# Performance work log

Hardware: AMD Instinct MI355X
Metric: run time of the kernel (lower is better)

## Reference

```python
import jax, jax.numpy as jnp
import numpy as np

K = 3            # kernel_size
ZETA = 1e-3      # crf_zeta
NUM_ITER = 2     # crf_num_iter
TOL = 0.0        # tolerance


def unfold3(x):
    """torch.nn.Unfold(3, stride=1, padding=1): [B,C,H,W] -> [B,C,9,H*W].
    Channel-major, kernel positions row-major (matches torch ordering)."""
    B, C, H, W = x.shape
    xp = jnp.pad(x, ((0, 0), (0, 0), (1, 1), (1, 1)))
    patches = jnp.stack(
        [xp[:, :, i:i + H, j:j + W] for i in range(K) for j in range(K)], axis=2
    )  # [B,C,9,H,W]
    return patches.reshape(B, C, K * K, H * W)


def setup_inputs() -> dict:
    key = jax.random.key(0)
    k1, k2, k3 = jax.random.split(key, 3)
    B, C, H, W, D = 2, 3, 256, 704, 64
    # scale color to O(zeta) so the gaussian affinity kernel is non-degenerate
    color = jax.random.normal(k1, (B, C, H, W), dtype=jnp.float32) * ZETA
    feats = jax.random.normal(k2, (B, C, H, W), dtype=jnp.float32)  # unused by forward, kept for signature fidelity
    logits = jax.random.normal(k3, (B, D, H, W), dtype=jnp.float32)
    ws = jnp.full((1,), 0.015, dtype=jnp.float32)  # learned weight self.ws[0]
    return {"color": color, "feats": feats, "logits": logits, "ws": ws}


def reference(color, feats, logits, ws):
    B, C, H, W = color.shape
    D = logits.shape[1]
    HW = H * W

    # gaussian affinity kernel from guide image: [B, 9, HW]
    uc = unfold3(color)  # [B,C,9,HW]
    kernel = jnp.exp(-(((uc - color.reshape(B, C, 1, HW)) ** 2)
                       / (2.0 * ZETA ** 2)).sum(1))

    # label compatibility matrix miu: [D, D]
    idx = jnp.arange(D)
    miu = jnp.clip(jnp.abs(idx[:, None] - idx[None, :]).astype(jnp.float32) - TOL, 0.0)

    logits_flat = logits.reshape(B, D, HW)
    q = jax.nn.softmax(logits, axis=1)
    for _ in range(NUM_ITER):
        uq = unfold3(q)  # [B,D,9,HW]
        q_tilde = (uq * kernel[:, None]).sum(2) * ws  # [B,D,HW]
        q_hat = jnp.einsum('de,ben->bdn', miu, q_tilde)  # [B,D,HW]
        q = jax.nn.softmax(logits_flat - q_hat, axis=1).reshape(B, D, H, W)
    return q
```

## Files before the change

kernel.cpp:

```cpp
#include <hip/hip_runtime.h>
#include <hip/hip_fp16.h>

#define HH 256
#define WW 704
#define DD 64
#define CC 3
#define BB 2
#define HWN (HH * WW)

#define TY 8
#define TX 16
#define RY0 12
#define RX0 20
#define NP0 (RY0 * RX0)
#define RY1 10
#define RX1 18
#define NP1 (RY1 * RX1)
#define NTX (WW / TX)
#define NTY (HH / TY)
#define NTILES (NTX * NTY)

static constexpr float INV2Z2 = 1.0f / (2.0f * 1e-3f * 1e-3f);
static constexpr float LOG2E  = 1.4426950408889634f;

__device__ __forceinline__ float fexp2(float x) {
#if __has_builtin(__builtin_amdgcn_exp2f)
    return __builtin_amdgcn_exp2f(x);
#else
    return __expf(x * 0.6931471805599453f);
#endif
}

__global__ __launch_bounds__(256) void affinity_kernel(
    const float* __restrict__ color, const float* __restrict__ wsp,
    float* __restrict__ kaffp)
{
    int n = blockIdx.x * 256 + threadIdx.x;
    int b = blockIdx.y;
    int h = n / WW, w = n - h * WW;
    float wsv = wsp[0] * LOG2E;

    const float* cb = color + (size_t)b * CC * HWN + n;
    float c0 = cb[0], c1 = cb[HWN], c2 = cb[2 * HWN];
    bool hm = h > 0, hp = h < HH - 1, wm = w > 0, wp = w < WW - 1;

    float kk[9];
#pragma unroll
    for (int dh = -1; dh <= 1; ++dh) {
#pragma unroll
        for (int dw = -1; dw <= 1; ++dw) {
            int k = (dh + 1) * 3 + (dw + 1);
            bool valid = (dh < 0 ? hm : (dh > 0 ? hp : true)) &&
                         (dw < 0 ? wm : (dw > 0 ? wp : true));
            int off = valid ? (dh * WW + dw) : 0;
            float u0 = valid ? cb[off] : 0.f;
            float u1 = valid ? cb[HWN + off] : 0.f;
            float u2 = valid ? cb[2 * HWN + off] : 0.f;
            float d0 = u0 - c0, d1 = u1 - c1, d2 = u2 - c2;
            float ss = d0 * d0 + d1 * d1 + d2 * d2;
            kk[k] = wsv * __expf(-ss * INV2Z2);
        }
    }
    float* kp = kaffp + ((size_t)b * HWN + n) * 12;
    *(float4*)(kp + 0) = make_float4(kk[0], kk[1], kk[2], kk[3]);
    *(float4*)(kp + 4) = make_float4(kk[4], kk[5], kk[6], kk[7]);
    *(float4*)(kp + 8) = make_float4(kk[8], 0.f, 0.f, 0.f);
}

__device__ __forceinline__ void acc_tap(const unsigned* q, int p0, int cg,
                                        __half2 kh, __half2* tv2) {
    int ia = p0 * 32 + ((cg * 8) ^ ((p0 & 7) << 2));
    int ib = ia ^ 4;
    const __half2* qa = (const __half2*)&q[ia];
    const __half2* qb = (const __half2*)&q[ib];
    tv2[0] = __hfma2(kh, qa[0], tv2[0]);
    tv2[1] = __hfma2(kh, qa[1], tv2[1]);
    tv2[2] = __hfma2(kh, qa[2], tv2[2]);
    tv2[3] = __hfma2(kh, qa[3], tv2[3]);
    tv2[4] = __hfma2(kh, qb[0], tv2[4]);
    tv2[5] = __hfma2(kh, qb[1], tv2[5]);
    tv2[6] = __hfma2(kh, qb[2], tv2[6]);
    tv2[7] = __hfma2(kh, qb[3], tv2[7]);
}

__device__ __forceinline__ void ld_raw(const unsigned* q, int p, int cg,
                                       uint4& a, uint4& bu) {
    int ia = p * 32 + ((cg * 8) ^ ((p & 7) << 2));
    a  = *(const uint4*)&q[ia];
    bu = *(const uint4*)&q[ia ^ 4];
}

__device__ __forceinline__ void unpack_px(uint4 a, uint4 bu, float* qc) {
    const __half2* pa = (const __half2*)&a;
    const __half2* pb = (const __half2*)&bu;
#pragma unroll
    for (int j = 0; j < 4; ++j) {
        float2 f = __half22float2(pa[j]);
        qc[2 * j] = f.x; qc[2 * j + 1] = f.y;
    }
#pragma unroll
    for (int j = 0; j < 4; ++j) {
        float2 f = __half22float2(pb[j]);
        qc[8 + 2 * j] = f.x; qc[8 + 2 * j + 1] = f.y;
    }
}

__device__ __forceinline__ void pack_px(const float* u, float scale,
                                        uint4& a, uint4& bu) {
    __half2* pa = (__half2*)&a;
    __half2* pb = (__half2*)&bu;
    pa[0] = __floats2half2_rn(u[0]  * scale, u[1]  * scale);
    pa[1] = __floats2half2_rn(u[2]  * scale, u[3]  * scale);
    pa[2] = __floats2half2_rn(u[4]  * scale, u[5]  * scale);
    pa[3] = __floats2half2_rn(u[6]  * scale, u[7]  * scale);
    pb[0] = __floats2half2_rn(u[8]  * scale, u[9]  * scale);
    pb[1] = __floats2half2_rn(u[10] * scale, u[11] * scale);
    pb[2] = __floats2half2_rn(u[12] * scale, u[13] * scale);
    pb[3] = __floats2half2_rn(u[14] * scale, u[15] * scale);
}

__device__ __forceinline__ void st_raw(unsigned* q, int p, int cg,
                                       uint4 a, uint4 bu) {
    int ia = p * 32 + ((cg * 8) ^ ((p & 7) << 2));
    *(uint4*)&q[ia] = a;
    *(uint4*)&q[ia ^ 4] = bu;
}

__device__ __forceinline__ void st_px(unsigned* q, int p, int cg,
                                      const float* u, float scale) {
    uint4 a, bu;
    pack_px(u, scale, a, bu);
    st_raw(q, p, cg, a, bu);
}

__device__ __forceinline__ void scan4(float Aloc, float Bloc, int pxl, int cg,
                                      float& Ar, float& Br, float& T, float& E) {
    float A0 = __shfl(Aloc, pxl),      A1 = __shfl(Aloc, pxl + 16),
          A2 = __shfl(Aloc, pxl + 32), A3 = __shfl(Aloc, pxl + 48);
    float B0 = __shfl(Bloc, pxl),      B1 = __shfl(Bloc, pxl + 16),
          B2 = __shfl(Bloc, pxl + 32), B3 = __shfl(Bloc, pxl + 48);
    T = A0 + A1 + A2 + A3;  E = B0 + B1 + B2 + B3;
    Ar = 0.f; Br = 0.f;
    if (cg > 0) { Ar += A0; Br += B0; }
    if (cg > 1) { Ar += A1; Br += B1; }
    if (cg > 2) { Ar += A2; Br += B2; }
}

__device__ __forceinline__ float finish_mult(float* tv, const float* qc,
                                             int pxl, int cg) {
    float Aloc = 0.f, Bloc = 0.f;
#pragma unroll
    for (int i = 0; i < 16; ++i) {
        float e = (float)(cg * 16 + i);
        Aloc += tv[i]; Bloc += e * tv[i];
    }
    float Ar, Br, T, E;
    scan4(Aloc, Bloc, pxl, cg, Ar, Br, T, E);
    float s = 0.f;
#pragma unroll
    for (int i = 0; i < 16; ++i) {
        float e = (float)(cg * 16 + i);
        Ar += tv[i]; Br += e * tv[i];
        float qh2 = 2.f * (e * Ar - Br) + E - e * T;
        tv[i] = qc[i] * fexp2(-qh2);
        s += tv[i];
    }
    s += __shfl_xor(s, 16);
    s += __shfl_xor(s, 32);
    return 1.f / s;
}

__device__ __forceinline__ void load_k(const float* kfbp, int n, int gy, int gx,
                                       float* k) {
    const float* kp = kfbp + (size_t)n * 12;
    float4 a = *(const float4*)(kp + 0);
    float4 bq = *(const float4*)(kp + 4);
    float4 c = *(const float4*)(kp + 8);
    k[0] = a.x; k[1] = a.y; k[2] = a.z; k[3] = a.w;
    k[4] = bq.x; k[5] = bq.y; k[6] = bq.z; k[7] = bq.w;
    k[8] = c.x;
    if (gy <= 0)      { k[0] = k[1] = k[2] = 0.f; }
    if (gy >= HH - 1) { k[6] = k[7] = k[8] = 0.f; }
    if (gx <= 0)      { k[0] = k[3] = k[6] = 0.f; }
    if (gx >= WW - 1) { k[2] = k[5] = k[8] = 0.f; }
}

__device__ __forceinline__ void stencil9(const unsigned* qs, int rowstride,
                                         int py, int px, int cg,
                                         const float* k, float* tv) {
    __half2 tv2[8];
#pragma unroll
    for (int j = 0; j < 8; ++j) tv2[j] = __float2half2_rn(0.f);
    int base = (py + 1) * rowstride + (px + 1);
#pragma unroll
    for (int tap = 0; tap < 9; ++tap) {
        int dy = tap / 3 - 1, dx = tap - (tap / 3) * 3 - 1;
        acc_tap(qs, base + dy * rowstride + dx, cg, __float2half2_rn(k[tap]), tv2);
    }
#pragma unroll
    for (int j = 0; j < 8; ++j) {
        float2 f = __half22float2(tv2[j]);
        tv[2 * j] = f.x; tv[2 * j + 1] = f.y;
    }
}

__global__ __launch_bounds__(512) void fused_crf_kernel(
    const float* __restrict__ logits, const float* __restrict__ kaffp,
    float* __restrict__ qout)
{
    __shared__ unsigned qs[NP0 * 32];

    const int t = threadIdx.x;
    const int lane = t & 63;
    const int wv = t >> 6;
    const int pxl = lane & 15;
    const int cg = lane >> 4;
    const int b = blockIdx.y;
    const int tid16 = wv * 16 + pxl;

    const int bid = blockIdx.x;
    const int pb = (bid & 7) * (NTILES / 8) + (bid >> 3);
    const int tyr = pb / NTX, txc = pb - tyr * NTX;
    const int y0 = tyr * TY, x0 = txc * TX;

    const float* lgb = logits + ((size_t)b * DD + cg * 16) * HWN;
    const float* kfbp = kaffp + (size_t)b * HWN * 12;

    for (int r = 0; r < 2; ++r) {
        int id = r * 128 + tid16;
        if (id < NP0) {
            int py = id / RX0, px = id - py * RX0;
            int gy = min(max(y0 - 2 + py, 0), HH - 1);
            int gx = min(max(x0 - 2 + px, 0), WW - 1);
            const float* lg = lgb + gy * WW + gx;
            float v[16];
            float s = 0.f;
#pragma unroll
            for (int i = 0; i < 16; ++i) {
                v[i] = __expf(lg[(size_t)i * HWN]);
                s += v[i];
            }
            s += __shfl_xor(s, 16);
            s += __shfl_xor(s, 32);
            st_px(qs, id, cg, v, 1.0f / s);
        }
    }
    __syncthreads();

    uint4 aA, buA;
    {
        int py = tid16 / RX1, px = tid16 - py * RX1;
        int gy = y0 - 1 + py, gx = x0 - 1 + px;
        int cy = min(max(gy, 0), HH - 1), cx = min(max(gx, 0), WW - 1);
        int n = cy * WW + cx;
        float k[9];
        load_k(kfbp, n, gy, gx, k);
        float tv[16];
        stencil9(qs, RX0, py, px, cg, k, tv);
        uint4 ca, cb2;
        ld_raw(qs, (py + 1) * RX0 + (px + 1), cg, ca, cb2);
        float qc[16];
        unpack_px(ca, cb2, qc);
        float inv = finish_mult(tv, qc, pxl, cg);
        pack_px(tv, inv, aA, buA);
    }
    const int idB = 128 + tid16;
    const bool validB = idB < NP1;
    uint4 aB, buB;
    if (validB) {
        int py = idB / RX1, px = idB - py * RX1;
        int gy = y0 - 1 + py, gx = x0 - 1 + px;
        int cy = min(max(gy, 0), HH - 1), cx = min(max(gx, 0), WW - 1);
        int n = cy * WW + cx;
        float k[9];
        load_k(kfbp, n, gy, gx, k);
        float tv[16];
        stencil9(qs, RX0, py, px, cg, k, tv);
        uint4 ca, cb2;
        ld_raw(qs, (py + 1) * RX0 + (px + 1), cg, ca, cb2);
        float qc[16];
        unpack_px(ca, cb2, qc);
        float inv = finish_mult(tv, qc, pxl, cg);
        pack_px(tv, inv, aB, buB);
    }

    uint4 q0cA, q0cB;
    {
        int pyc = tid16 >> 4, pxc = tid16 & 15;
        ld_raw(qs, (pyc + 2) * RX0 + (pxc + 2), cg, q0cA, q0cB);
    }
    __syncthreads();

    st_raw(qs, tid16, cg, aA, buA);
    if (validB) st_raw(qs, idB, cg, aB, buB);
    __syncthreads();

    {
        int py = tid16 >> 4, px = tid16 & 15;
        int gy = y0 + py, gx = x0 + px;
        int n = gy * WW + gx;

        float k[9];
        load_k(kfbp, n, gy, gx, k);

        float tv[16];
        stencil9(qs, RX1, py, px, cg, k, tv);
        float qc[16];
        unpack_px(q0cA, q0cB, qc);
        float inv = finish_mult(tv, qc, pxl, cg);

        float* qo = qout + ((size_t)b * DD + cg * 16) * HWN + n;
#pragma unroll
        for (int i = 0; i < 16; ++i) qo[(size_t)i * HWN] = tv[i] * inv;
    }
}

extern "C" void kernel_launch(void* const* d_in, const int* in_sizes, int n_in,
                              void* d_out, int out_size, void* d_ws, size_t ws_size,
                              hipStream_t stream) {
    const float* color  = (const float*)d_in[0];
    const float* logits = (const float*)d_in[2];
    const float* wsp    = (const float*)d_in[3];

    float* q_out = (float*)d_out;
    float* kaffp = (float*)d_ws;

    dim3 gridA(HWN / 256, BB);
    affinity_kernel<<<gridA, 256, 0, stream>>>(color, wsp, kaffp);

    dim3 gridF(NTILES, BB);
    fused_crf_kernel<<<gridF, 512, 0, stream>>>(logits, kaffp, q_out);
}
```

Before: 80.21 us.

## Double fused CRF tile height to cut halo recomputation

The tile grows from 8x16 to 16x16 output pixels, so the softmax of the 2-pixel halo and the first-iteration stencil over the 1-pixel halo are recomputed for a smaller share of pixels. Both loops are restructured to cover more rows: four rounds of softmax loading, three rounds of the first mean-field iteration, and two output rounds. First-iteration results are now written back into shared memory in place, one round at a time, with a barrier between rounds; the centre q values are cached in registers beforehand. The trade-off is roughly 51KB of LDS per block instead of 30KB, half as many blocks, more barriers and higher register pressure, all of which can lower occupancy.

```diff
diff --git a/kernel.cpp b/kernel.cpp
--- a/kernel.cpp
+++ b/kernel.cpp
@@ -8,12 +8,12 @@
 #define BB 2
 #define HWN (HH * WW)
 
-#define TY 8
+#define TY 16
 #define TX 16
-#define RY0 12
+#define RY0 20
 #define RX0 20
 #define NP0 (RY0 * RX0)
-#define RY1 10
+#define RY1 18
 #define RX1 18
 #define NP1 (RY1 * RX1)
 #define NTX (WW / TX)
@@ -226,7 +226,7 @@
     const float* lgb = logits + ((size_t)b * DD + cg * 16) * HWN;
     const float* kfbp = kaffp + (size_t)b * HWN * 12;
 
-    for (int r = 0; r < 2; ++r) {
+    for (int r = 0; r < 4; ++r) {
         int id = r * 128 + tid16;
         if (id < NP0) {
             int py = id / RX0, px = id - py * RX0;
@@ -247,56 +247,45 @@
     }
     __syncthreads();
 
-    uint4 aA, buA;
-    {
-        int py = tid16 / RX1, px = tid16 - py * RX1;
-        int gy = y0 - 1 + py, gx = x0 - 1 + px;
-        int cy = min(max(gy, 0), HH - 1), cx = min(max(gx, 0), WW - 1);
-        int n = cy * WW + cx;
-        float k[9];
-        load_k(kfbp, n, gy, gx, k);
-        float tv[16];
-        stencil9(qs, RX0, py, px, cg, k, tv);
-        uint4 ca, cb2;
-        ld_raw(qs, (py + 1) * RX0 + (px + 1), cg, ca, cb2);
-        float qc[16];
-        unpack_px(ca, cb2, qc);
-        float inv = finish_mult(tv, qc, pxl, cg);
-        pack_px(tv, inv, aA, buA);
-    }
-    const int idB = 128 + tid16;
-    const bool validB = idB < NP1;
-    uint4 aB, buB;
-    if (validB) {
-        int py = idB / RX1, px = idB - py * RX1;
-        int gy = y0 - 1 + py, gx = x0 - 1 + px;
-        int cy = min(max(gy, 0), HH - 1), cx = min(max(gx, 0), WW - 1);
-        int n = cy * WW + cx;
-        float k[9];
-        load_k(kfbp, n, gy, gx, k);
-        float tv[16];
-        stencil9(qs, RX0, py, px, cg, k, tv);
-        uint4 ca, cb2;
-        ld_raw(qs, (py + 1) * RX0 + (px + 1), cg, ca, cb2);
-        float qc[16];
-        unpack_px(ca, cb2, qc);
-        float inv = finish_mult(tv, qc, pxl, cg);
-        pack_px(tv, inv, aB, buB);
-    }
-
-    uint4 q0cA, q0cB;
-    {
-        int pyc = tid16 >> 4, pxc = tid16 & 15;
-        ld_raw(qs, (pyc + 2) * RX0 + (pxc + 2), cg, q0cA, q0cB);
-    }
-    __syncthreads();
-
-    st_raw(qs, tid16, cg, aA, buA);
-    if (validB) st_raw(qs, idB, cg, aB, buB);
-    __syncthreads();
-
+    uint4 s0a, s0b, s1a, s1b;
     {
         int py = tid16 >> 4, px = tid16 & 15;
+        ld_raw(qs, (py + 2) * RX0 + (px + 2), cg, s0a, s0b);
+        int id2 = 128 + tid16;
+        int py2 = id2 >> 4, px2 = id2 & 15;
+        ld_raw(qs, (py2 + 2) * RX0 + (px2 + 2), cg, s1a, s1b);
+    }
+
+#pragma unroll
+    for (int r = 0; r < 3; ++r) {
+        int id = r * 128 + tid16;
+        bool valid = (r < 2) || (id < NP1);
+        uint4 a, bu;
+        if (valid) {
+            int py = id / RX1, px = id - py * RX1;
+            int gy = y0 - 1 + py, gx = x0 - 1 + px;
+            int cy = min(max(gy, 0), HH - 1), cx = min(max(gx, 0), WW - 1);
+            int n = cy * WW + cx;
+            float k[9];
+            load_k(kfbp, n, gy, gx, k);
+            float tv[16];
+            stencil9(qs, RX0, py, px, cg, k, tv);
+            uint4 ca, cb2;
+            ld_raw(qs, (py + 1) * RX0 + (px + 1), cg, ca, cb2);
+            float qc[16];
+            unpack_px(ca, cb2, qc);
+            float inv = finish_mult(tv, qc, pxl, cg);
+            pack_px(tv, inv, a, bu);
+        }
+        __syncthreads();
+        if (valid) st_raw(qs, id, cg, a, bu);
+    }
+    __syncthreads();
+
+#pragma unroll
+    for (int r = 0; r < 2; ++r) {
+        int id = r * 128 + tid16;
+        int py = id >> 4, px = id & 15;
         int gy = y0 + py, gx = x0 + px;
         int n = gy * WW + gx;
 
@@ -306,7 +295,7 @@
         float tv[16];
         stencil9(qs, RX1, py, px, cg, k, tv);
         float qc[16];
-        unpack_px(q0cA, q0cB, qc);
+        unpack_px(r == 0 ? s0a : s1a, r == 0 ? s0b : s1b, qc);
         float inv = finish_mult(tv, qc, pxl, cg);
 
         float* qo = qout + ((size_t)b * DD + cg * 16) * HWN + n;
```

After: 83.17 us. 1.04x slower.
